# Optimization experiments

Measured on AMD Instinct MI355X. Metric: run time of the kernel, lower is better.

The kernel has to match this reference:

```python
import jax, jax.numpy as jnp
import numpy as np

B, S, D = 2048, 200, 64
H1, H2 = 64, 16
EPS = 1e-9
NEG_INF = -2.0**32 + 1.0


def dice(x, alpha, mean, var):
    # Dice activation at inference: BN (no center/scale) with moving stats, then
    # p = sigmoid(x_norm); out = alpha*(1-p)*x + p*x
    xn = (x - mean) * jax.lax.rsqrt(var + EPS)
    p = jax.nn.sigmoid(xn)
    return alpha * (1.0 - p) * x + p * x


def setup_inputs() -> dict:
    key = jax.random.key(0)
    ks = jax.random.split(key, 12)
    query_emb = jax.random.normal(ks[0], (B, D), dtype=jnp.float32)
    key_emb = jax.random.normal(ks[1], (B, S, D), dtype=jnp.float32)
    seq_length = jax.random.randint(ks[2], (B, 1), 1, S + 1, dtype=jnp.int32)
    # attention MLP weights (no bias): 4*D -> H1 -> H2 -> 1
    W1 = jax.random.normal(ks[3], (4 * D, H1), dtype=jnp.float32) * 0.05
    W2 = jax.random.normal(ks[4], (H1, H2), dtype=jnp.float32) * 0.05
    W3 = jax.random.normal(ks[5], (H2, 1), dtype=jnp.float32) * 0.05
    # Dice params: alpha (trainable) + BN moving stats
    alpha1 = jax.random.normal(ks[6], (H1,), dtype=jnp.float32) * 0.1
    mean1 = jax.random.normal(ks[7], (H1,), dtype=jnp.float32) * 0.1
    var1 = jax.random.uniform(ks[8], (H1,), dtype=jnp.float32, minval=0.5, maxval=1.5)
    alpha2 = jax.random.normal(ks[9], (H2,), dtype=jnp.float32) * 0.1
    mean2 = jax.random.normal(ks[10], (H2,), dtype=jnp.float32) * 0.1
    var2 = jax.random.uniform(ks[11], (H2,), dtype=jnp.float32, minval=0.5, maxval=1.5)
    return {
        "query_emb": query_emb, "key_emb": key_emb, "seq_length": seq_length,
        "W1": W1, "alpha1": alpha1, "mean1": mean1, "var1": var1,
        "W2": W2, "alpha2": alpha2, "mean2": mean2, "var2": var2,
        "W3": W3,
    }


def reference(query_emb, key_emb, seq_length, W1, alpha1, mean1, var1,
              W2, alpha2, mean2, var2, W3):
    b, s, d = key_emb.shape
    q = jnp.broadcast_to(query_emb[:, None, :], (b, s, d))
    # (B, S, 4D) interaction features
    att = jnp.concatenate([q, key_emb, q - key_emb, q * key_emb], axis=-1)
    h = dice(att @ W1, alpha1, mean1, var1)           # (B, S, H1)
    h = dice(h @ W2, alpha2, mean2, var2)             # (B, S, H2)
    score = h @ W3                                    # (B, S, 1)
    mask = (jnp.arange(s)[None, :] < seq_length).astype(score.dtype)[..., None]
    score = score * mask + (1.0 - mask) * NEG_INF
    score = jax.nn.sigmoid(score)                     # weight_normalization=False
    return jnp.sum(score * key_emb, axis=1)           # (B, D)
```

## Files before the change

kernel.cpp:

```cpp
#include <hip/hip_runtime.h>

#define NB   2048
#define SEQ  200
#define DIM  64
#define NH1  64
#define NH2  16
#define EPSF 1e-9f

typedef float fvec4 __attribute__((ext_vector_type(4)));
typedef short svec8 __attribute__((ext_vector_type(8)));

#define SMEM_BYTES 17920

__device__ __forceinline__ short f2bf(float f) {
    unsigned u = __float_as_uint(f);
    u += 0x7fffu + ((u >> 16) & 1u);
    return (short)(u >> 16);
}

__global__ __launch_bounds__(256, 4)
void din_attn_kernel(const float* __restrict__ q,
                     const float* __restrict__ key,
                     const int*   __restrict__ seqlen,
                     const float* __restrict__ W1,
                     const float* __restrict__ alpha1v,
                     const float* __restrict__ mean1v,
                     const float* __restrict__ var1v,
                     const float* __restrict__ W2,
                     const float* __restrict__ alpha2v,
                     const float* __restrict__ mean2v,
                     const float* __restrict__ var2v,
                     const float* __restrict__ W3,
                     float* __restrict__ out)
{
    __shared__ __align__(16) char smem[SMEM_BYTES];
    float* wc_t  = (float*)(smem);
    float* qpart = (float*)(smem + 16384);
    float* outp  = (float*)(smem + 16384);
    float* qall  = (float*)(smem + 17408);
    float* wshb  = (float*)(smem + 17664);

    const int b    = blockIdx.x;
    const int t    = threadIdx.x;
    const int lane = t & 63;
    const int wave = __builtin_amdgcn_readfirstlane(t >> 6);
    const int qd4  = lane >> 4;
    const int m    = lane & 15;

    short* h1w = (short*)(smem + wave * 2048);
    float* wsw = wshb + wave * 16;

    const float* qrow = q + (size_t)b * DIM;
    int nseq = seqlen[b];
    nseq = nseq < SEQ ? nseq : SEQ;

    {
        const int h = lane;
        float qt = 0.f;
        #pragma unroll
        for (int i = 0; i < 16; ++i) {
            const int d = wave * 16 + i;
            const float qdv  = qrow[d];
            const float w1a  = W1[(d)       * NH1 + h];
            const float w1b  = W1[(64 + d)  * NH1 + h];
            const float w1c  = W1[(128 + d) * NH1 + h];
            const float w1dd = W1[(192 + d) * NH1 + h];
            wc_t[d * NH1 + h] = (w1b - w1c) + qdv * w1dd;
            qt = fmaf(qdv, w1a + w1c, qt);
        }
        qpart[wave * 64 + h] = qt;
    }
    __syncthreads();

    if (t < 64)
        qall[t] = (qpart[t] + qpart[64 + t]) + (qpart[128 + t] + qpart[192 + t]);

    svec8 wcf[4][2];
    #pragma unroll
    for (int c = 0; c < 4; ++c)
        #pragma unroll
        for (int kk = 0; kk < 2; ++kk) {
            svec8 f;
            #pragma unroll
            for (int j = 0; j < 8; ++j) {
                const int d = kk * 32 + qd4 * 8 + j;
                f[j] = f2bf(wc_t[d * NH1 + (c * 16 + m)]);
            }
            wcf[c][kk] = f;
        }

    svec8 w2f[2];
    #pragma unroll
    for (int kk = 0; kk < 2; ++kk) {
        svec8 f;
        #pragma unroll
        for (int j = 0; j < 8; ++j) {
            const int h = kk * 32 + qd4 * 8 + j;
            f[j] = f2bf(W2[h * NH2 + m]);
        }
        w2f[kk] = f;
    }

    float a1v[4], m1v[4], r1v[4];
    #pragma unroll
    for (int c = 0; c < 4; ++c) {
        a1v[c] = alpha1v[c * 16 + m];
        m1v[c] = mean1v[c * 16 + m];
        r1v[c] = rsqrtf(var1v[c * 16 + m] + EPSF);
    }
    const float a2s = alpha2v[m];
    const float m2s = mean2v[m];
    const float r2s = rsqrtf(var2v[m] + EPSF);
    const float w3s = W3[m];

    __syncthreads();

    float qtermv[4];
    #pragma unroll
    for (int c = 0; c < 4; ++c) qtermv[c] = qall[c * 16 + m];

    fvec4 oacc0 = {0.f,0.f,0.f,0.f}, oacc1 = {0.f,0.f,0.f,0.f};
    fvec4 oacc2 = {0.f,0.f,0.f,0.f}, oacc3 = {0.f,0.f,0.f,0.f};

    const int ntiles = (nseq + 15) >> 4;
    for (int tile = wave; tile < ntiles; tile += 4) {
        const int row  = tile * 16 + m;
        const int grow = row < SEQ ? row : SEQ - 1;
        const float* kp = key + ((size_t)b * SEQ + grow) * DIM + qd4 * 8;
        const fvec4 kv0 = *(const fvec4*)(kp);
        const fvec4 kv1 = *(const fvec4*)(kp + 4);
        const fvec4 kv2 = *(const fvec4*)(kp + 32);
        const fvec4 kv3 = *(const fvec4*)(kp + 36);

        svec8 af0, af1;
        #pragma unroll
        for (int j = 0; j < 4; ++j) {
            af0[j]     = f2bf(kv0[j]);
            af0[4 + j] = f2bf(kv1[j]);
            af1[j]     = f2bf(kv2[j]);
            af1[4 + j] = f2bf(kv3[j]);
        }

        fvec4 acc[4];
        #pragma unroll
        for (int c = 0; c < 4; ++c) {
            acc[c] = (fvec4){0.f, 0.f, 0.f, 0.f};
            acc[c] = __builtin_amdgcn_mfma_f32_16x16x32_bf16(af0, wcf[c][0], acc[c], 0, 0, 0);
            acc[c] = __builtin_amdgcn_mfma_f32_16x16x32_bf16(af1, wcf[c][1], acc[c], 0, 0, 0);
        }

        #pragma unroll
        for (int c = 0; c < 4; ++c) {
            #pragma unroll
            for (int reg = 0; reg < 4; ++reg) {
                const float x  = acc[c][reg] + qtermv[c];
                const float xn = (x - m1v[c]) * r1v[c];
                const float p  = 1.f / (1.f + __expf(-xn));
                const float h1 = x * (a1v[c] + p * (1.f - a1v[c]));
                h1w[(qd4 * 4 + reg) * NH1 + c * 16 + m] = f2bf(h1);
            }
        }

        const svec8 b0 = *(const svec8*)(h1w + m * NH1 + qd4 * 8);
        const svec8 b1 = *(const svec8*)(h1w + m * NH1 + 32 + qd4 * 8);
        fvec4 acc2 = (fvec4){0.f, 0.f, 0.f, 0.f};
        acc2 = __builtin_amdgcn_mfma_f32_16x16x32_bf16(b0, w2f[0], acc2, 0, 0, 0);
        acc2 = __builtin_amdgcn_mfma_f32_16x16x32_bf16(b1, w2f[1], acc2, 0, 0, 0);

        #pragma unroll
        for (int reg = 0; reg < 4; ++reg) {
            const float x  = acc2[reg];
            const float xn = (x - m2s) * r2s;
            const float p  = 1.f / (1.f + __expf(-xn));
            const float hd = x * (a2s + p * (1.f - a2s));
            float s = hd * w3s;
            s += __shfl_xor(s, 1);
            s += __shfl_xor(s, 2);
            s += __shfl_xor(s, 4);
            s += __shfl_xor(s, 8);
            if (m == 0) {
                const int rg = tile * 16 + qd4 * 4 + reg;
                wsw[qd4 * 4 + reg] = (rg < nseq) ? 1.f / (1.f + __expf(-s)) : 0.f;
            }
        }

        const float w = wsw[m];
        oacc0 += w * kv0;
        oacc1 += w * kv1;
        oacc2 += w * kv2;
        oacc3 += w * kv3;
    }

    #pragma unroll
    for (int e = 0; e < 4; ++e) {
        float v0 = oacc0[e], v1 = oacc1[e], v2 = oacc2[e], v3 = oacc3[e];
        #pragma unroll
        for (int msk = 1; msk < 16; msk <<= 1) {
            v0 += __shfl_xor(v0, msk);
            v1 += __shfl_xor(v1, msk);
            v2 += __shfl_xor(v2, msk);
            v3 += __shfl_xor(v3, msk);
        }
        oacc0[e] = v0; oacc1[e] = v1; oacc2[e] = v2; oacc3[e] = v3;
    }
    if (m == 0) {
        #pragma unroll
        for (int e = 0; e < 4; ++e) {
            outp[wave * 64 + qd4 * 8 + e]          = oacc0[e];
            outp[wave * 64 + qd4 * 8 + 4 + e]      = oacc1[e];
            outp[wave * 64 + 32 + qd4 * 8 + e]     = oacc2[e];
            outp[wave * 64 + 32 + qd4 * 8 + 4 + e] = oacc3[e];
        }
    }
    __syncthreads();

    if (t < 64) {
        out[(size_t)b * DIM + t] = (outp[t] + outp[64 + t]) +
                                   (outp[128 + t] + outp[192 + t]);
    }
}

extern "C" void kernel_launch(void* const* d_in, const int* in_sizes, int n_in,
                              void* d_out, int out_size, void* d_ws, size_t ws_size,
                              hipStream_t stream) {
    const float* q      = (const float*)d_in[0];
    const float* key    = (const float*)d_in[1];
    const int*   seqlen = (const int*)d_in[2];
    const float* W1     = (const float*)d_in[3];
    const float* alpha1 = (const float*)d_in[4];
    const float* mean1  = (const float*)d_in[5];
    const float* var1   = (const float*)d_in[6];
    const float* W2     = (const float*)d_in[7];
    const float* alpha2 = (const float*)d_in[8];
    const float* mean2  = (const float*)d_in[9];
    const float* var2   = (const float*)d_in[10];
    const float* W3     = (const float*)d_in[11];
    float* out          = (float*)d_out;

    din_attn_kernel<<<NB, 256, 0, stream>>>(q, key, seqlen, W1,
                                            alpha1, mean1, var1,
                                            W2, alpha2, mean2, var2,
                                            W3, out);
}
```

Baseline: 188.2 us.

## Split per-query weight prep into separate kernel and use one-wave main blocks

Moves the per-batch folding of W1 with the query into a prep kernel that writes bf16 MFMA fragments and query terms to workspace. Each prep block handles four rows so the W1 combination is built once per block. The main kernel becomes one wave per batch row, which drops the block syncs and cross-wave reduction, and it software-prefetches the next key tile into registers. The cost is an extra launch, a round trip of about 16 MB through workspace, and less parallelism per row with serial tiles.

```diff
diff --git a/kernel.cpp b/kernel.cpp
--- a/kernel.cpp
+++ b/kernel.cpp
@@ -6,11 +6,10 @@
 #define NH1  64
 #define NH2  16
 #define EPSF 1e-9f
+#define ROWS1 4
 
 typedef float fvec4 __attribute__((ext_vector_type(4)));
 typedef short svec8 __attribute__((ext_vector_type(8)));
-
-#define SMEM_BYTES 17920
 
 __device__ __forceinline__ short f2bf(float f) {
     unsigned u = __float_as_uint(f);
@@ -18,86 +17,113 @@
     return (short)(u >> 16);
 }
 
-__global__ __launch_bounds__(256, 4)
-void din_attn_kernel(const float* __restrict__ q,
-                     const float* __restrict__ key,
+__global__ __launch_bounds__(256, 2)
+void din_prep_kernel(const float* __restrict__ q,
+                     const float* __restrict__ W1,
+                     char*  __restrict__ wsA,
+                     float* __restrict__ qtermws)
+{
+    __shared__ float Wsub[4096];
+    __shared__ float Wd[4096];
+    __shared__ float Wac[4096];
+    const int t = threadIdx.x;
+
+    #pragma unroll
+    for (int it = 0; it < 16; ++it) {
+        const int e = it * 256 + t;
+        const int d = e >> 6, h = e & 63;
+        const float w1a = W1[d * 64 + h];
+        const float w1b = W1[(64 + d) * 64 + h];
+        const float w1c = W1[(128 + d) * 64 + h];
+        const float w1dv= W1[(192 + d) * 64 + h];
+        Wsub[e] = w1b - w1c;
+        Wac[e]  = w1a + w1c;
+        Wd[e]   = w1dv;
+    }
+    __syncthreads();
+
+    const int lane = t & 63;
+    const int wave = t >> 6;
+    const int qd4  = lane >> 4;
+    const int m    = lane & 15;
+
+    for (int r = 0; r < ROWS1; ++r) {
+        const int b = blockIdx.x * ROWS1 + r;
+        const float* qrow = q + (size_t)b * DIM;
+
+        {
+            const int h = wave * 16 + m;
+            float s = 0.f;
+            #pragma unroll
+            for (int i = 0; i < 16; ++i) {
+                const int d = qd4 * 16 + i;
+                s = fmaf(qrow[d], Wac[d * 64 + h], s);
+            }
+            s += __shfl_xor(s, 16);
+            s += __shfl_xor(s, 32);
+            if (qd4 == 0) qtermws[(size_t)b * 64 + h] = s;
+        }
+
+        #pragma unroll
+        for (int kk = 0; kk < 2; ++kk) {
+            svec8 f;
+            #pragma unroll
+            for (int j = 0; j < 8; ++j) {
+                const int d = kk * 32 + qd4 * 8 + j;
+                const int h = wave * 16 + m;
+                f[j] = f2bf(Wsub[d * 64 + h] + qrow[d] * Wd[d * 64 + h]);
+            }
+            *(svec8*)(wsA + (size_t)b * 8192 + (((wave << 1) + kk) << 10) + lane * 16) = f;
+        }
+    }
+}
+
+__global__ __launch_bounds__(64, 2)
+void din_main_kernel(const float* __restrict__ key,
                      const int*   __restrict__ seqlen,
-                     const float* __restrict__ W1,
+                     const float* __restrict__ W2,
                      const float* __restrict__ alpha1v,
                      const float* __restrict__ mean1v,
                      const float* __restrict__ var1v,
-                     const float* __restrict__ W2,
                      const float* __restrict__ alpha2v,
                      const float* __restrict__ mean2v,
                      const float* __restrict__ var2v,
                      const float* __restrict__ W3,
+                     const char*  __restrict__ wsA,
+                     const float* __restrict__ qtermws,
                      float* __restrict__ out)
 {
-    __shared__ __align__(16) char smem[SMEM_BYTES];
-    float* wc_t  = (float*)(smem);
-    float* qpart = (float*)(smem + 16384);
-    float* outp  = (float*)(smem + 16384);
-    float* qall  = (float*)(smem + 17408);
-    float* wshb  = (float*)(smem + 17664);
+    __shared__ short h1w[16 * NH1];
+    __shared__ float wsw[16];
 
     const int b    = blockIdx.x;
-    const int t    = threadIdx.x;
-    const int lane = t & 63;
-    const int wave = __builtin_amdgcn_readfirstlane(t >> 6);
+    const int lane = threadIdx.x;
     const int qd4  = lane >> 4;
     const int m    = lane & 15;
 
-    short* h1w = (short*)(smem + wave * 2048);
-    float* wsw = wshb + wave * 16;
-
-    const float* qrow = q + (size_t)b * DIM;
     int nseq = seqlen[b];
     nseq = nseq < SEQ ? nseq : SEQ;
 
+    svec8 wcf[4][2];
     {
-        const int h = lane;
-        float qt = 0.f;
-        #pragma unroll
-        for (int i = 0; i < 16; ++i) {
-            const int d = wave * 16 + i;
-            const float qdv  = qrow[d];
-            const float w1a  = W1[(d)       * NH1 + h];
-            const float w1b  = W1[(64 + d)  * NH1 + h];
-            const float w1c  = W1[(128 + d) * NH1 + h];
-            const float w1dd = W1[(192 + d) * NH1 + h];
-            wc_t[d * NH1 + h] = (w1b - w1c) + qdv * w1dd;
-            qt = fmaf(qdv, w1a + w1c, qt);
-        }
-        qpart[wave * 64 + h] = qt;
-    }
-    __syncthreads();
-
-    if (t < 64)
-        qall[t] = (qpart[t] + qpart[64 + t]) + (qpart[128 + t] + qpart[192 + t]);
-
-    svec8 wcf[4][2];
-    #pragma unroll
-    for (int c = 0; c < 4; ++c)
-        #pragma unroll
-        for (int kk = 0; kk < 2; ++kk) {
-            svec8 f;
-            #pragma unroll
-            for (int j = 0; j < 8; ++j) {
-                const int d = kk * 32 + qd4 * 8 + j;
-                f[j] = f2bf(wc_t[d * NH1 + (c * 16 + m)]);
-            }
-            wcf[c][kk] = f;
-        }
+        const char* fb = wsA + (size_t)b * 8192 + (size_t)lane * 16;
+        #pragma unroll
+        for (int c = 0; c < 4; ++c)
+            #pragma unroll
+            for (int kk = 0; kk < 2; ++kk)
+                wcf[c][kk] = *(const svec8*)(fb + (((c << 1) + kk) << 10));
+    }
+    float qtermv[4];
+    #pragma unroll
+    for (int c = 0; c < 4; ++c) qtermv[c] = qtermws[(size_t)b * 64 + c * 16 + m];
 
     svec8 w2f[2];
     #pragma unroll
     for (int kk = 0; kk < 2; ++kk) {
         svec8 f;
         #pragma unroll
-        for (int j = 0; j < 8; ++j) {
-            const int h = kk * 32 + qd4 * 8 + j;
-            f[j] = f2bf(W2[h * NH2 + m]);
-        }
+        for (int j = 0; j < 8; ++j)
+            f[j] = f2bf(W2[(kk * 32 + qd4 * 8 + j) * NH2 + m]);
         w2f[kk] = f;
     }
 
@@ -113,24 +139,32 @@
     const float r2s = rsqrtf(var2v[m] + EPSF);
     const float w3s = W3[m];
 
-    __syncthreads();
-
-    float qtermv[4];
-    #pragma unroll
-    for (int c = 0; c < 4; ++c) qtermv[c] = qall[c * 16 + m];
-
     fvec4 oacc0 = {0.f,0.f,0.f,0.f}, oacc1 = {0.f,0.f,0.f,0.f};
     fvec4 oacc2 = {0.f,0.f,0.f,0.f}, oacc3 = {0.f,0.f,0.f,0.f};
 
     const int ntiles = (nseq + 15) >> 4;
-    for (int tile = wave; tile < ntiles; tile += 4) {
-        const int row  = tile * 16 + m;
-        const int grow = row < SEQ ? row : SEQ - 1;
-        const float* kp = key + ((size_t)b * SEQ + grow) * DIM + qd4 * 8;
-        const fvec4 kv0 = *(const fvec4*)(kp);
-        const fvec4 kv1 = *(const fvec4*)(kp + 4);
-        const fvec4 kv2 = *(const fvec4*)(kp + 32);
-        const fvec4 kv3 = *(const fvec4*)(kp + 36);
+    const float* kbase = key + (size_t)b * SEQ * DIM + qd4 * 8;
+
+    fvec4 nv0, nv1, nv2, nv3;
+    {
+        const float* kp = kbase + (size_t)m * DIM;
+        nv0 = *(const fvec4*)(kp);
+        nv1 = *(const fvec4*)(kp + 4);
+        nv2 = *(const fvec4*)(kp + 32);
+        nv3 = *(const fvec4*)(kp + 36);
+    }
+
+    for (int tile = 0; tile < ntiles; ++tile) {
+        const fvec4 kv0 = nv0, kv1 = nv1, kv2 = nv2, kv3 = nv3;
+        if (tile + 1 < ntiles) {
+            int row = (tile + 1) * 16 + m;
+            row = row < SEQ ? row : SEQ - 1;
+            const float* kp = kbase + (size_t)row * DIM;
+            nv0 = *(const fvec4*)(kp);
+            nv1 = *(const fvec4*)(kp + 4);
+            nv2 = *(const fvec4*)(kp + 32);
+            nv3 = *(const fvec4*)(kp + 36);
+        }
 
         svec8 af0, af1;
         #pragma unroll
@@ -141,19 +175,14 @@
             af1[4 + j] = f2bf(kv3[j]);
         }
 
-        fvec4 acc[4];
         #pragma unroll
         for (int c = 0; c < 4; ++c) {
-            acc[c] = (fvec4){0.f, 0.f, 0.f, 0.f};
-            acc[c] = __builtin_amdgcn_mfma_f32_16x16x32_bf16(af0, wcf[c][0], acc[c], 0, 0, 0);
-            acc[c] = __builtin_amdgcn_mfma_f32_16x16x32_bf16(af1, wcf[c][1], acc[c], 0, 0, 0);
-        }
-
-        #pragma unroll
-        for (int c = 0; c < 4; ++c) {
+            fvec4 acc = (fvec4){0.f, 0.f, 0.f, 0.f};
+            acc = __builtin_amdgcn_mfma_f32_16x16x32_bf16(af0, wcf[c][0], acc, 0, 0, 0);
+            acc = __builtin_amdgcn_mfma_f32_16x16x32_bf16(af1, wcf[c][1], acc, 0, 0, 0);
             #pragma unroll
             for (int reg = 0; reg < 4; ++reg) {
-                const float x  = acc[c][reg] + qtermv[c];
+                const float x  = acc[reg] + qtermv[c];
                 const float xn = (x - m1v[c]) * r1v[c];
                 const float p  = 1.f / (1.f + __expf(-xn));
                 const float h1 = x * (a1v[c] + p * (1.f - a1v[c]));
@@ -204,19 +233,11 @@
         oacc0[e] = v0; oacc1[e] = v1; oacc2[e] = v2; oacc3[e] = v3;
     }
     if (m == 0) {
-        #pragma unroll
-        for (int e = 0; e < 4; ++e) {
-            outp[wave * 64 + qd4 * 8 + e]          = oacc0[e];
-            outp[wave * 64 + qd4 * 8 + 4 + e]      = oacc1[e];
-            outp[wave * 64 + 32 + qd4 * 8 + e]     = oacc2[e];
-            outp[wave * 64 + 32 + qd4 * 8 + 4 + e] = oacc3[e];
-        }
-    }
-    __syncthreads();
-
-    if (t < 64) {
-        out[(size_t)b * DIM + t] = (outp[t] + outp[64 + t]) +
-                                   (outp[128 + t] + outp[192 + t]);
+        float* op = out + (size_t)b * DIM + qd4 * 8;
+        *(fvec4*)(op)      = oacc0;
+        *(fvec4*)(op + 4)  = oacc1;
+        *(fvec4*)(op + 32) = oacc2;
+        *(fvec4*)(op + 36) = oacc3;
     }
 }
 
@@ -237,8 +258,12 @@
     const float* W3     = (const float*)d_in[11];
     float* out          = (float*)d_out;
 
-    din_attn_kernel<<<NB, 256, 0, stream>>>(q, key, seqlen, W1,
-                                            alpha1, mean1, var1,
-                                            W2, alpha2, mean2, var2,
-                                            W3, out);
-}
+    char*  wsA     = (char*)d_ws;
+    float* qtermws = (float*)((char*)d_ws + (size_t)NB * 8192);
+
+    din_prep_kernel<<<NB / ROWS1, 256, 0, stream>>>(q, W1, wsA, qtermws);
+    din_main_kernel<<<NB, 64, 0, stream>>>(key, seqlen, W2,
+                                           alpha1, mean1, var1,
+                                           alpha2, mean2, var2,
+                                           W3, wsA, qtermws, out);
+}
```

New measurement: 192.3 us. 1.02x slower.
